# Performance work log

Measured on AMD Instinct MI355X. Metric: run time of the kernel, lower is better.

The kernel has to match this reference:

```python
import jax, jax.numpy as jnp
import numpy as np

B, L, W, C = 16, 200, 64, 128
H_INTRA = 64   # intra_hidden // 2 per direction
H_INTER = 128
EPS = 1e-8


def layer_norm(x, gamma, beta):
    mu = jnp.mean(x, axis=-1, keepdims=True)
    var = jnp.mean(jnp.square(x - mu), axis=-1, keepdims=True)
    return (x - mu) * jax.lax.rsqrt(var + EPS) * gamma + beta


def gru_seq(x, Wk, Uk, b, H):
    """Keras GRU, reset_after=False, recurrent_activation=sigmoid. x: [N,T,D] -> [N,T,H]."""
    xw = jnp.einsum('ntd,dk->ntk', x, Wk) + b  # precompute input projections [N,T,3H]
    def step(h, xw_t):
        z = jax.nn.sigmoid(xw_t[:, :H] + h @ Uk[:, :H])
        r = jax.nn.sigmoid(xw_t[:, H:2 * H] + h @ Uk[:, H:2 * H])
        hh = jnp.tanh(xw_t[:, 2 * H:] + (r * h) @ Uk[:, 2 * H:])
        h = z * h + (1.0 - z) * hh
        return h, h
    h0 = jnp.zeros((x.shape[0], H), x.dtype)
    _, ys = jax.lax.scan(step, h0, jnp.swapaxes(xw, 0, 1))  # [T,N,H]
    return jnp.swapaxes(ys, 0, 1)


def skip_gru_seq(x, Wk, Uk, b, Wp, bp, H):
    """Skip-RNN GRU (Campos et al.): binary update gate u_t conditionally updates state.
    Returns (outputs [N,T,H], gates [N,T,1])."""
    xw = jnp.einsum('ntd,dk->ntk', x, Wk) + b
    def step(carry, xw_t):
        h, ut = carry
        # straight-through binarization of cumulative update prob
        u = ut + jax.lax.stop_gradient(jnp.round(ut) - ut)  # [N,1]
        z = jax.nn.sigmoid(xw_t[:, :H] + h @ Uk[:, :H])
        r = jax.nn.sigmoid(xw_t[:, H:2 * H] + h @ Uk[:, H:2 * H])
        hh = jnp.tanh(xw_t[:, 2 * H:] + (r * h) @ Uk[:, 2 * H:])
        h_new = z * h + (1.0 - z) * hh
        h = u * h_new + (1.0 - u) * h  # skip: copy state when u == 0
        delta = jax.nn.sigmoid(h @ Wp + bp)  # [N,1]
        ut_next = u * delta + (1.0 - u) * (ut + jnp.minimum(delta, 1.0 - ut))
        return (h, ut_next), (h, u)
    N = x.shape[0]
    h0 = jnp.zeros((N, H), x.dtype)
    ut0 = jnp.ones((N, 1), x.dtype)
    _, (ys, us) = jax.lax.scan(step, (h0, ut0), jnp.swapaxes(xw, 0, 1))
    return jnp.swapaxes(ys, 0, 1), jnp.swapaxes(us, 0, 1)


def setup_inputs():
    key = jax.random.key(0)
    ks = jax.random.split(key, 16)
    rn = lambda k, s: jax.random.normal(k, s, dtype=jnp.float32) * 0.05
    z = lambda s: jnp.zeros(s, jnp.float32)
    o = lambda s: jnp.ones(s, jnp.float32)
    return {
        'x': jax.random.normal(ks[0], (B, L, W, C), dtype=jnp.float32),
        'scale': jax.random.uniform(ks[1], (B, L, W, 1), dtype=jnp.float32),
        'Wf': rn(ks[2], (C, 3 * H_INTRA)), 'Uf': rn(ks[3], (H_INTRA, 3 * H_INTRA)), 'bf': z((3 * H_INTRA,)),
        'Wb': rn(ks[4], (C, 3 * H_INTRA)), 'Ub': rn(ks[5], (H_INTRA, 3 * H_INTRA)), 'bb': z((3 * H_INTRA,)),
        'W_intra_fc': rn(ks[6], (2 * H_INTRA, C)), 'b_intra_fc': z((C,)),
        'g_intra': o((C,)), 'beta_intra': z((C,)),
        'Wi': rn(ks[7], (C + 1, 3 * H_INTER)), 'Ui': rn(ks[8], (H_INTER, 3 * H_INTER)), 'bi': z((3 * H_INTER,)),
        'Wp': rn(ks[9], (H_INTER, 1)), 'bp': z((1,)),
        'W_inter_fc': rn(ks[10], (H_INTER, C)), 'b_inter_fc': z((C,)),
        'g_inter': o((C,)), 'beta_inter': z((C,)),
    }


def reference(x, scale, Wf, Uf, bf, Wb, Ub, bb, W_intra_fc, b_intra_fc, g_intra, beta_intra,
              Wi, Ui, bi, Wp, bp, W_inter_fc, b_inter_fc, g_inter, beta_inter):
    # ----- intra path: bidirectional GRU over the width axis -----
    intra_in = x.reshape(B * L, W, C)
    out_f = gru_seq(intra_in, Wf, Uf, bf, H_INTRA)
    out_b = gru_seq(intra_in[:, ::-1, :], Wb, Ub, bb, H_INTRA)[:, ::-1, :]
    intra_rnn_out = jnp.concatenate([out_f, out_b], axis=-1)  # [B*L, W, 2H]
    update_gate_intra = jnp.ones((64, L), jnp.float32)  # skip=0 branch: constant ones
    intra_dense = intra_rnn_out @ W_intra_fc + b_intra_fc  # [B*L, W, C]
    intra_out = x + layer_norm(intra_dense.reshape(B, L, W, C), g_intra, beta_intra)
    # ----- inter path: skip-GRU over the L (time) axis -----
    inter_in = jnp.transpose(intra_out, (0, 2, 1, 3)).reshape(B * W, L, C)
    scale2 = jnp.transpose(scale, (0, 2, 1, 3)).reshape(B * W, L, 1)
    inter_in = jnp.concatenate([inter_in, scale2], axis=-1)  # [B*W, L, C+1]
    inter_rnn_out, gates = skip_gru_seq(inter_in, Wi, Ui, bi, Wp, bp, H_INTER)
    update_gate_inter = gates[:, :, 0]  # [B*W, L]
    inter_dense = (inter_rnn_out @ W_inter_fc + b_inter_fc).reshape(B, W, L, C)
    inter_ln_in = jnp.transpose(inter_dense, (0, 2, 1, 3))  # [B, L, W, C]
    inter_out = intra_out + layer_norm(inter_ln_in, g_inter, beta_inter)
    return inter_out, update_gate_intra, update_gate_inter
```

## Files before the change

kernel.cpp:

```cpp
#include <hip/hip_runtime.h>
#include <cmath>


typedef float f32x16 __attribute__((ext_vector_type(16)));

__device__ __forceinline__ float sigf(float x) { return 1.0f / (1.0f + expf(-x)); }
__device__ __forceinline__ float rlanef(float v, int l) {
  return __uint_as_float(__builtin_amdgcn_readlane(__float_as_uint(v), (unsigned)l));
}

template <int SB>
__device__ __forceinline__ void macP2(const f32x16& u0, const f32x16& u1, float hv,
                                      float& a0, float& a1) {
#pragma unroll
  for (int k = 0; k < 16; ++k) {
    const float hs = rlanef(hv, SB + k);
    a0 = fmaf(u0[k], hs, a0);
    a1 = fmaf(u1[k], hs, a1);
  }
}
template <int SB>
__device__ __forceinline__ void macP1(const f32x16& u, float hv, float& a) {
#pragma unroll
  for (int k = 0; k < 16; ++k) a = fmaf(u[k], rlanef(hv, SB + k), a);
}

__global__ __launch_bounds__(256) void k_fill_ones(float* __restrict__ p, int n) {
  int i = blockIdx.x * 256 + threadIdx.x;
  if (i < n) p[i] = 1.0f;
}

enum { MA_X_FWD = 0, MA_X_BWD = 1, MA_INTER = 2 };

template <int MODE>
__global__ __launch_bounds__(256) void k_gemm_xw(
    const float* __restrict__ A0, const float* __restrict__ A1,
    const float* __restrict__ Bm, const float* __restrict__ bias,
    float* __restrict__ Cm, long M0, int N, int K, int KT)
{
  __shared__ float As[16][68];
  __shared__ float Bs[16][68];
  const int tid = threadIdx.x;
  const int tx = tid & 15, ty = tid >> 4;
  const long row0g = M0 + (long)blockIdx.x * 64;
  const int col0 = blockIdx.y * 64;
  const int lr = tid >> 2;
  const int lk4 = (tid & 3) * 4;
  const int bk = tid >> 4;
  const int bc4 = (tid & 15) * 4;
  float acc[4][4];
#pragma unroll
  for (int i = 0; i < 4; ++i)
#pragma unroll
    for (int j = 0; j < 4; ++j) acc[i][j] = 0.f;

  for (int kt = 0; kt < KT; ++kt) {
    const int k0 = kt * 16;
    {
      const long rg = row0g + lr;
      float v0, v1, v2, v3;
      if (MODE == MA_X_FWD) {
        const float4 a4 = *reinterpret_cast<const float4*>(&A0[rg * 128 + k0 + lk4]);
        v0 = a4.x; v1 = a4.y; v2 = a4.z; v3 = a4.w;
      } else if (MODE == MA_X_BWD) {
        const long s = rg >> 6; const int t = (int)(rg & 63);
        const float4 a4 =
            *reinterpret_cast<const float4*>(&A0[(s * 64 + (63 - t)) * 128 + k0 + lk4]);
        v0 = a4.x; v1 = a4.y; v2 = a4.z; v3 = a4.w;
      } else {
        const int n = (int)(rg & 1023);
        const int l = (int)(rg >> 10);
        const long rowc = ((long)(n >> 6) * 200 + l) * 64 + (n & 63);
        const long base = rowc * 128;
        if (kt < 8) {
          const float4 a4 = *reinterpret_cast<const float4*>(&A0[base + k0 + lk4]);
          v0 = a4.x; v1 = a4.y; v2 = a4.z; v3 = a4.w;
        } else {
          v0 = (lk4 == 0) ? A1[rowc] : 0.f;
          v1 = 0.f; v2 = 0.f; v3 = 0.f;
        }
      }
      As[lk4 + 0][lr] = v0;
      As[lk4 + 1][lr] = v1;
      As[lk4 + 2][lr] = v2;
      As[lk4 + 3][lr] = v3;
    }
    {
      const int k = k0 + bk;
      float4 b4 = make_float4(0.f, 0.f, 0.f, 0.f);
      if (k < K) b4 = *reinterpret_cast<const float4*>(&Bm[(long)k * N + col0 + bc4]);
      *reinterpret_cast<float4*>(&Bs[bk][bc4]) = b4;
    }
    __syncthreads();
#pragma unroll
    for (int kk = 0; kk < 16; ++kk) {
      const float4 a4 = *reinterpret_cast<const float4*>(&As[kk][ty * 4]);
      const float4 b4 = *reinterpret_cast<const float4*>(&Bs[kk][tx * 4]);
      const float av[4] = {a4.x, a4.y, a4.z, a4.w};
      const float bv[4] = {b4.x, b4.y, b4.z, b4.w};
#pragma unroll
      for (int i = 0; i < 4; ++i)
#pragma unroll
        for (int j = 0; j < 4; ++j) acc[i][j] = fmaf(av[i], bv[j], acc[i][j]);
    }
    __syncthreads();
  }
  const float4 bi4 = *reinterpret_cast<const float4*>(&bias[col0 + tx * 4]);
  const float bv[4] = {bi4.x, bi4.y, bi4.z, bi4.w};
#pragma unroll
  for (int i = 0; i < 4; ++i) {
    const long rl = (long)blockIdx.x * 64 + ty * 4 + i;
    float4 o;
    o.x = acc[i][0] + bv[0];
    o.y = acc[i][1] + bv[1];
    o.z = acc[i][2] + bv[2];
    o.w = acc[i][3] + bv[3];
    *reinterpret_cast<float4*>(&Cm[rl * (long)N + col0 + tx * 4]) = o;
  }
}

__global__ __launch_bounds__(256, 4) void k_gru_intra4(
    const float* __restrict__ xwf, const float* __restrict__ xwb,
    const float* __restrict__ Uf, const float* __restrict__ Ub,
    float* __restrict__ rnn)
{
  const int dir = blockIdx.y;
  const float* __restrict__ xw = dir ? xwb : xwf;
  const float* __restrict__ U  = dir ? Ub : Uf;
  __shared__ float h8[4][64], z8[4][64], rh8[4][64];
  __shared__ float pA[4][4][128];
  __shared__ float pB[4][4][64];
  const int tid = threadIdx.x;
  const int w = tid >> 6, lane = tid & 63;
  const long s0 = (long)blockIdx.x * 4;

  f32x16 uz, ur, uhh;
#pragma unroll
  for (int k = 0; k < 16; ++k) {
    const int row = (w * 16 + k) * 192;
    uz[k]  = U[row + lane];
    ur[k]  = U[row + 64 + lane];
    uhh[k] = U[row + 128 + lane];
  }
  h8[w][lane] = 0.f;
  __syncthreads();

  const long xrow0 = (s0 + w) * 64;
  float xa1 = xw[xrow0 * 192 + lane];
  float xa2 = xw[xrow0 * 192 + 64 + lane];
  float xb  = xw[xrow0 * 192 + 128 + lane];

  for (int t = 0; t < 64; ++t) {
    const int tn = (t < 63) ? t + 1 : t;
    const float xa1n = xw[(xrow0 + tn) * 192 + lane];
    const float xa2n = xw[(xrow0 + tn) * 192 + 64 + lane];
    const float xbn  = xw[(xrow0 + tn) * 192 + 128 + lane];
    {
      const float hv01 = h8[lane >> 5][w * 16 + (lane & 15)];
      const float hv23 = h8[2 + (lane >> 5)][w * 16 + (lane & 15)];
      float az0 = 0.f, ar0 = 0.f, az1 = 0.f, ar1 = 0.f;
      float az2 = 0.f, ar2 = 0.f, az3 = 0.f, ar3 = 0.f;
      macP2<0>(uz, ur, hv01, az0, ar0);
      macP2<32>(uz, ur, hv01, az1, ar1);
      macP2<0>(uz, ur, hv23, az2, ar2);
      macP2<32>(uz, ur, hv23, az3, ar3);
      pA[0][w][lane] = az0; pA[0][w][64 + lane] = ar0;
      pA[1][w][lane] = az1; pA[1][w][64 + lane] = ar1;
      pA[2][w][lane] = az2; pA[2][w][64 + lane] = ar2;
      pA[3][w][lane] = az3; pA[3][w][64 + lane] = ar3;
    }
    __syncthreads();
    {
      const float sz = pA[w][0][lane] + pA[w][1][lane] + pA[w][2][lane] +
                       pA[w][3][lane] + xa1;
      const float sr = pA[w][0][64 + lane] + pA[w][1][64 + lane] +
                       pA[w][2][64 + lane] + pA[w][3][64 + lane] + xa2;
      z8[w][lane] = sigf(sz);
      rh8[w][lane] = sigf(sr) * h8[w][lane];
    }
    __syncthreads();
    {
      const float rv01 = rh8[lane >> 5][w * 16 + (lane & 15)];
      const float rv23 = rh8[2 + (lane >> 5)][w * 16 + (lane & 15)];
      float a0 = 0.f, a1 = 0.f, a2 = 0.f, a3 = 0.f;
      macP1<0>(uhh, rv01, a0);
      macP1<32>(uhh, rv01, a1);
      macP1<0>(uhh, rv23, a2);
      macP1<32>(uhh, rv23, a3);
      pB[0][w][lane] = a0;
      pB[1][w][lane] = a1;
      pB[2][w][lane] = a2;
      pB[3][w][lane] = a3;
    }
    __syncthreads();
    {
      const float pre = pB[w][0][lane] + pB[w][1][lane] + pB[w][2][lane] +
                        pB[w][3][lane] + xb;
      const float hh = tanhf(pre);
      const float z = z8[w][lane];
      const float ho = h8[w][lane];
      const float hn = z * ho + (1.f - z) * hh;
      h8[w][lane] = hn;
      const int tt = dir ? (63 - t) : t;
      rnn[((s0 + w) * 64 + tt) * 128 + dir * 64 + lane] = hn;
    }
    __syncthreads();
    xa1 = xa1n; xa2 = xa2n; xb = xbn;
  }
}

__global__ __launch_bounds__(1024, 4) void k_gru_inter5(
    const float* __restrict__ xw, const float* __restrict__ Ui,
    const float* __restrict__ Wp, const float* __restrict__ bp,
    float* __restrict__ rnn, float* __restrict__ gates,
    float* __restrict__ hstate, float* __restrict__ ustate,
    int t0, int nt)
{
  __shared__ float h4[4][128], z4[4][128], rh4[4][128];
  __shared__ float pA[4][8][256];
  __shared__ float pB[4][8][128];
  __shared__ float uu[4], utt[4];
  const int tid = threadIdx.x;
  const int w = tid >> 6, lane = tid & 63;
  const int n0 = blockIdx.x * 4;
  const int kA = (w & 7) * 16;
  const int cH = w >> 3;

  f32x16 uzA, uzB, uh;
#pragma unroll
  for (int k = 0; k < 16; ++k) {
    const long r = (long)(kA + k) * 384;
    uzA[k] = Ui[r + cH * 128 + lane];
    uzB[k] = Ui[r + cH * 128 + 64 + lane];
    uh[k]  = Ui[r + 256 + cH * 64 + lane];
  }
  if (tid < 512) {
    const int s = tid >> 7, c = tid & 127;
    h4[s][c] = (t0 == 0) ? 0.f : hstate[(long)(n0 + s) * 128 + c];
  }
  if (tid < 4) {
    utt[tid] = (t0 == 0) ? 1.f : ustate[n0 + tid];
    uu[tid]  = (t0 == 0) ? 1.f : ustate[1024 + n0 + tid];
  }
  const float bp0 = bp[0];
  float wprA = 0.f, wprB = 0.f;
  if (w < 4) { wprA = Wp[lane]; wprB = Wp[64 + lane]; }
  __syncthreads();

  const int sC = tid >> 8;
  const int cC = tid & 255;
  float xc = xw[(long)(n0 + sC) * 384 + cC];
  float xbA = 0.f, xbB = 0.f;
  if (w < 4) {
    xbA = xw[(long)(n0 + w) * 384 + 256 + lane];
    xbB = xw[(long)(n0 + w) * 384 + 320 + lane];
  }

  for (int dl = 0; dl < nt; ++dl) {
    const float u0g = uu[0], u1g = uu[1], u2g = uu[2], u3g = uu[3];
    const bool act = (u0g + u1g + u2g + u3g) != 0.f;
    const int dn = (dl + 1 < nt) ? dl + 1 : dl;
    const float xcn = xw[((long)dn * 1024 + n0 + sC) * 384 + cC];
    float xbAn = 0.f, xbBn = 0.f;
    if (w < 4) {
      xbAn = xw[((long)dn * 1024 + n0 + w) * 384 + 256 + lane];
      xbBn = xw[((long)dn * 1024 + n0 + w) * 384 + 320 + lane];
    }
    if (act) {
      {
        const float hv01 = h4[lane >> 5][kA + (lane & 15)];
        const float hv23 = h4[2 + (lane >> 5)][kA + (lane & 15)];
        const int kq = w & 7;
        if (u0g != 0.f) {
          float a0 = 0.f, a1 = 0.f;
          macP2<0>(uzA, uzB, hv01, a0, a1);
          pA[0][kq][cH * 128 + lane] = a0;
          pA[0][kq][cH * 128 + 64 + lane] = a1;
        }
        if (u1g != 0.f) {
          float a0 = 0.f, a1 = 0.f;
          macP2<32>(uzA, uzB, hv01, a0, a1);
          pA[1][kq][cH * 128 + lane] = a0;
          pA[1][kq][cH * 128 + 64 + lane] = a1;
        }
        if (u2g != 0.f) {
          float a0 = 0.f, a1 = 0.f;
          macP2<0>(uzA, uzB, hv23, a0, a1);
          pA[2][kq][cH * 128 + lane] = a0;
          pA[2][kq][cH * 128 + 64 + lane] = a1;
        }
        if (u3g != 0.f) {
          float a0 = 0.f, a1 = 0.f;
          macP2<32>(uzA, uzB, hv23, a0, a1);
          pA[3][kq][cH * 128 + lane] = a0;
          pA[3][kq][cH * 128 + 64 + lane] = a1;
        }
      }
      __syncthreads();
      {
        if (uu[sC] != 0.f) {
          float sum = xc;
#pragma unroll
          for (int q = 0; q < 8; ++q) sum += pA[sC][q][cC];
          if (cC < 128) z4[sC][cC] = sigf(sum);
          else rh4[sC][cC - 128] = sigf(sum) * h4[sC][cC - 128];
        }
      }
      __syncthreads();
      {
        const float rv01 = rh4[lane >> 5][kA + (lane & 15)];
        const float rv23 = rh4[2 + (lane >> 5)][kA + (lane & 15)];
        const int kq = w & 7;
        if (u0g != 0.f) {
          float b = 0.f; macP1<0>(uh, rv01, b);
          pB[0][kq][cH * 64 + lane] = b;
        }
        if (u1g != 0.f) {
          float b = 0.f; macP1<32>(uh, rv01, b);
          pB[1][kq][cH * 64 + lane] = b;
        }
        if (u2g != 0.f) {
          float b = 0.f; macP1<0>(uh, rv23, b);
          pB[2][kq][cH * 64 + lane] = b;
        }
        if (u3g != 0.f) {
          float b = 0.f; macP1<32>(uh, rv23, b);
          pB[3][kq][cH * 64 + lane] = b;
        }
      }
      __syncthreads();
    }
    if (w < 4) {
      const float us = uu[w];
      const float hoA = h4[w][lane], hoB = h4[w][64 + lane];
      float hqA, hqB;
      if (us != 0.f) {
        float sA = xbA, sB = xbB;
#pragma unroll
        for (int q = 0; q < 8; ++q) {
          sA += pB[w][q][lane];
          sB += pB[w][q][64 + lane];
        }
        const float hhA = tanhf(sA), hhB = tanhf(sB);
        const float zA = z4[w][lane], zB = z4[w][64 + lane];
        hqA = zA * hoA + (1.f - zA) * hhA;
        hqB = zB * hoB + (1.f - zB) * hhB;
        h4[w][lane] = hqA;
        h4[w][64 + lane] = hqB;
      } else {
        hqA = hoA; hqB = hoB;
      }
      rnn[((long)dl * 1024 + n0 + w) * 128 + lane] = hqA;
      rnn[((long)dl * 1024 + n0 + w) * 128 + 64 + lane] = hqB;
      float p = hqA * wprA + hqB * wprB;
      p += __shfl_xor(p, 32);
      p += __shfl_xor(p, 16);
      p += __shfl_xor(p, 8);
      p += __shfl_xor(p, 4);
      p += __shfl_xor(p, 2);
      p += __shfl_xor(p, 1);
      const float delta = sigf(p + bp0);
      const float ut = utt[w];
      const float utn = us * delta + (1.f - us) * (ut + fminf(delta, 1.f - ut));
      if (lane == 0) {
        gates[(long)(n0 + w) * 200 + t0 + dl] = us;
        utt[w] = utn;
        uu[w] = rintf(utn);
      }
    }
    __syncthreads();
    xc = xcn; xbA = xbAn; xbB = xbBn;
  }
  if (tid < 512) {
    const int s = tid >> 7, c = tid & 127;
    hstate[(long)(n0 + s) * 128 + c] = h4[s][c];
  }
  if (tid < 4) {
    ustate[n0 + tid] = utt[tid];
    ustate[1024 + n0 + tid] = uu[tid];
  }
}

template <int OM>
__global__ __launch_bounds__(256) void k_fcln(
    const float* __restrict__ A, const float* __restrict__ Wt,
    const float* __restrict__ bias, const float* __restrict__ gamma,
    const float* __restrict__ beta, const float* __restrict__ resid,
    float* __restrict__ dst, long M0)
{
  __shared__ float As[16][36];
  __shared__ float Bs[16][132];
  __shared__ float red0[32][33];
  __shared__ float red1[32][33];
  __shared__ float mu_s[32];
  __shared__ float rs_s[32];
  const int tid = threadIdx.x;
  const int tx = tid & 31, ty = tid >> 5;
  const long r0l = (long)blockIdx.x * 32;
  const int lr = tid >> 3;
  const int lk2 = (tid & 7) * 2;
  const int bkk = tid >> 4;
  const int bc8 = (tid & 15) * 8;
  float acc[4][4];
#pragma unroll
  for (int i = 0; i < 4; ++i)
#pragma unroll
    for (int j = 0; j < 4; ++j) acc[i][j] = 0.f;

  for (int kt = 0; kt < 8; ++kt) {
    const int k0 = kt * 16;
    const float2 a2 = *reinterpret_cast<const float2*>(&A[(r0l + lr) * 128 + k0 + lk2]);
    As[lk2][lr] = a2.x;
    As[lk2 + 1][lr] = a2.y;
    const float4 w0 = *reinterpret_cast<const float4*>(&Wt[(long)(k0 + bkk) * 128 + bc8]);
    const float4 w1 = *reinterpret_cast<const float4*>(&Wt[(long)(k0 + bkk) * 128 + bc8 + 4]);
    *reinterpret_cast<float4*>(&Bs[bkk][bc8]) = w0;
    *reinterpret_cast<float4*>(&Bs[bkk][bc8 + 4]) = w1;
    __syncthreads();
#pragma unroll
    for (int kk = 0; kk < 16; ++kk) {
      const float4 a4 = *reinterpret_cast<const float4*>(&As[kk][ty * 4]);
      const float4 b4 = *reinterpret_cast<const float4*>(&Bs[kk][tx * 4]);
      const float av[4] = {a4.x, a4.y, a4.z, a4.w};
      const float bv[4] = {b4.x, b4.y, b4.z, b4.w};
#pragma unroll
      for (int i = 0; i < 4; ++i)
#pragma unroll
        for (int j = 0; j < 4; ++j) acc[i][j] = fmaf(av[i], bv[j], acc[i][j]);
    }
    __syncthreads();
  }
  {
    const float4 bb4 = *reinterpret_cast<const float4*>(&bias[tx * 4]);
    const float bv[4] = {bb4.x, bb4.y, bb4.z, bb4.w};
#pragma unroll
    for (int i = 0; i < 4; ++i)
#pragma unroll
      for (int j = 0; j < 4; ++j) acc[i][j] += bv[j];
  }
#pragma unroll
  for (int i = 0; i < 4; ++i) {
    const float s = acc[i][0] + acc[i][1] + acc[i][2] + acc[i][3];
    const float q = acc[i][0] * acc[i][0] + acc[i][1] * acc[i][1] +
                    acc[i][2] * acc[i][2] + acc[i][3] * acc[i][3];
    red0[ty * 4 + i][tx] = s;
    red1[ty * 4 + i][tx] = q;
  }
  __syncthreads();
  if (tid < 32) {
    float s = 0.f, q = 0.f;
#pragma unroll
    for (int j = 0; j < 32; ++j) { s += red0[tid][j]; q += red1[tid][j]; }
    const float mu = s * (1.0f / 128.0f);
    const float var = q * (1.0f / 128.0f) - mu * mu;
    mu_s[tid] = mu;
    rs_s[tid] = 1.0f / sqrtf(var + 1e-8f);
  }
  __syncthreads();
  const float4 g4 = *reinterpret_cast<const float4*>(&gamma[tx * 4]);
  const float4 be4 = *reinterpret_cast<const float4*>(&beta[tx * 4]);
#pragma unroll
  for (int i = 0; i < 4; ++i) {
    const int rloc = ty * 4 + i;
    const long rg = M0 + r0l + rloc;
    long off;
    if (OM == 0) {
      off = rg * 128 + tx * 4;
    } else {
      const int n = (int)(rg & 1023);
      const int l = (int)(rg >> 10);
      off = (((long)(n >> 6) * 200 + l) * 64 + (n & 63)) * 128 + tx * 4;
    }
    const float4 r4 = *reinterpret_cast<const float4*>(&resid[off]);
    const float mu = mu_s[rloc], rs = rs_s[rloc];
    float4 o;
    o.x = (acc[i][0] - mu) * rs * g4.x + be4.x + r4.x;
    o.y = (acc[i][1] - mu) * rs * g4.y + be4.y + r4.y;
    o.z = (acc[i][2] - mu) * rs * g4.z + be4.z + r4.z;
    o.w = (acc[i][3] - mu) * rs * g4.w + be4.w + r4.w;
    *reinterpret_cast<float4*>(&dst[off]) = o;
  }
}

extern "C" void kernel_launch(void* const* d_in, const int* in_sizes, int n_in,
                              void* d_out, int out_size, void* d_ws, size_t ws_size,
                              hipStream_t stream)
{
  (void)in_sizes; (void)n_in; (void)out_size;
  const float* x    = (const float*)d_in[0];
  const float* scl  = (const float*)d_in[1];
  const float* Wf   = (const float*)d_in[2];
  const float* Uf   = (const float*)d_in[3];
  const float* bf   = (const float*)d_in[4];
  const float* Wb   = (const float*)d_in[5];
  const float* Ub   = (const float*)d_in[6];
  const float* bb   = (const float*)d_in[7];
  const float* Wfc1 = (const float*)d_in[8];
  const float* bfc1 = (const float*)d_in[9];
  const float* gam1 = (const float*)d_in[10];
  const float* bet1 = (const float*)d_in[11];
  const float* Wi   = (const float*)d_in[12];
  const float* Ui   = (const float*)d_in[13];
  const float* bi   = (const float*)d_in[14];
  const float* Wp   = (const float*)d_in[15];
  const float* bp   = (const float*)d_in[16];
  const float* Wfc2 = (const float*)d_in[17];
  const float* bfc2 = (const float*)d_in[18];
  const float* gam2 = (const float*)d_in[19];
  const float* bet2 = (const float*)d_in[20];

  float* outp  = (float*)d_out;
  float* io    = outp;
  float* onesp = outp + 26214400L;
  float* gates = outp + 26214400L + 12800L;
  float* ws    = (float*)d_ws;
  const long wsf = (long)(ws_size / sizeof(float));

  k_fill_ones<<<50, 256, 0, stream>>>(onesp, 12800);

  long cnI = (wsf / 32768L) & ~7L;
  if (cnI > 3200) cnI = 3200;
  if (cnI < 8) cnI = 8;
  for (long s0 = 0; s0 < 3200; s0 += cnI) {
    const long cn = (3200 - s0 < cnI) ? (3200 - s0) : cnI;
    float* xwf = ws;
    float* xwb = ws + cn * 12288L;
    float* rnn = ws + cn * 24576L;
    const long M = cn * 64;
    dim3 gg((unsigned)(M / 64), 3);
    k_gemm_xw<MA_X_FWD><<<gg, 256, 0, stream>>>(x, nullptr, Wf, bf, xwf, s0 * 64, 192, 128, 8);
    k_gemm_xw<MA_X_BWD><<<gg, 256, 0, stream>>>(x, nullptr, Wb, bb, xwb, s0 * 64, 192, 128, 8);
    dim3 gr((unsigned)(cn / 4), 2);
    k_gru_intra4<<<gr, 256, 0, stream>>>(xwf, xwb, Uf, Ub, rnn);
    k_fcln<0><<<(unsigned)(M / 32), 256, 0, stream>>>(rnn, Wfc1, bfc1, gam1, bet1, x, io, s0 * 64);
  }

  const long per_t = 1024L * 384 + 1024L * 128;
  const long state_f = 1024L * 128 + 3072L;
  long nt_alloc = (wsf - state_f) / per_t;
  if (nt_alloc > 200) nt_alloc = 200;
  if (nt_alloc < 1) nt_alloc = 1;
  float* xwi    = ws;
  float* rnnI   = ws + nt_alloc * 1024L * 384;
  float* hstate = rnnI + nt_alloc * 1024L * 128;
  float* ustate = hstate + 1024L * 128;

  for (long t0 = 0; t0 < 200; t0 += nt_alloc) {
    const int nt = (int)((200 - t0 < nt_alloc) ? (200 - t0) : nt_alloc);
    dim3 gg((unsigned)(16 * nt), 6);
    k_gemm_xw<MA_INTER><<<gg, 256, 0, stream>>>(io, scl, Wi, bi, xwi, t0 * 1024, 384, 129, 9);
    k_gru_inter5<<<256, 1024, 0, stream>>>(xwi, Ui, Wp, bp, rnnI, gates, hstate, ustate,
                                           (int)t0, nt);
    k_fcln<1><<<(unsigned)(32 * nt), 256, 0, stream>>>(rnnI, Wfc2, bfc2, gam2, bet2, io, outp,
                                                       t0 * 1024);
  }
}
```

Measured before the change: 1.792 ms.

## Split inter skip-GRU across 512 blocks of two sequences and widen GEMM K-tile

The inter skip-GRU kernel now handles 2 sequences per 1024-thread block instead of 4, launching 512 blocks. Each wave owns 8 rows of the recurrent matrix across all output columns, and partial sums are reduced over 16 waves. This spreads the serial recurrence over twice as many CUs to cut per-step latency, at the cost of more shared-memory reduction work and a larger register footprint per thread. Separately, the input-projection GEMM moves from a 16-wide to a 32-wide K tile, halving the number of barrier-separated iterations, and its address computation is hoisted out of the K loop.

```diff
diff --git a/kernel.cpp b/kernel.cpp
--- a/kernel.cpp
+++ b/kernel.cpp
@@ -2,29 +2,13 @@
 #include <cmath>
 
 
-typedef float f32x16 __attribute__((ext_vector_type(16)));
+typedef float f32x8 __attribute__((ext_vector_type(8)));
 
 __device__ __forceinline__ float sigf(float x) { return 1.0f / (1.0f + expf(-x)); }
 __device__ __forceinline__ float rlanef(float v, int l) {
   return __uint_as_float(__builtin_amdgcn_readlane(__float_as_uint(v), (unsigned)l));
 }
 
-template <int SB>
-__device__ __forceinline__ void macP2(const f32x16& u0, const f32x16& u1, float hv,
-                                      float& a0, float& a1) {
-#pragma unroll
-  for (int k = 0; k < 16; ++k) {
-    const float hs = rlanef(hv, SB + k);
-    a0 = fmaf(u0[k], hs, a0);
-    a1 = fmaf(u1[k], hs, a1);
-  }
-}
-template <int SB>
-__device__ __forceinline__ void macP1(const f32x16& u, float hv, float& a) {
-#pragma unroll
-  for (int k = 0; k < 16; ++k) a = fmaf(u[k], rlanef(hv, SB + k), a);
-}
-
 __global__ __launch_bounds__(256) void k_fill_ones(float* __restrict__ p, int n) {
   int i = blockIdx.x * 256 + threadIdx.x;
   if (i < n) p[i] = 1.0f;
@@ -33,13 +17,13 @@
 enum { MA_X_FWD = 0, MA_X_BWD = 1, MA_INTER = 2 };
 
 template <int MODE>
-__global__ __launch_bounds__(256) void k_gemm_xw(
+__global__ __launch_bounds__(256, 6) void k_gemm_xw(
     const float* __restrict__ A0, const float* __restrict__ A1,
     const float* __restrict__ Bm, const float* __restrict__ bias,
     float* __restrict__ Cm, long M0, int N, int K, int KT)
 {
-  __shared__ float As[16][68];
-  __shared__ float Bs[16][68];
+  __shared__ float As[32][68];
+  __shared__ float Bs[32][68];
   const int tid = threadIdx.x;
   const int tx = tid & 15, ty = tid >> 4;
   const long row0g = M0 + (long)blockIdx.x * 64;
@@ -54,46 +38,54 @@
 #pragma unroll
     for (int j = 0; j < 4; ++j) acc[i][j] = 0.f;
 
+  const long rg = row0g + lr;
+  long abase = 0;
+  long rowc = 0;
+  if (MODE == MA_X_FWD) {
+    abase = rg * 128;
+  } else if (MODE == MA_X_BWD) {
+    const long s = rg >> 6; const int t = (int)(rg & 63);
+    abase = (s * 64 + (63 - t)) * 128;
+  } else {
+    const int n = (int)(rg & 1023);
+    const int l = (int)(rg >> 10);
+    rowc = ((long)(n >> 6) * 200 + l) * 64 + (n & 63);
+    abase = rowc * 128;
+  }
+
   for (int kt = 0; kt < KT; ++kt) {
-    const int k0 = kt * 16;
-    {
-      const long rg = row0g + lr;
+    const int k0 = kt * 32;
+#pragma unroll
+    for (int half = 0; half < 32; half += 16) {
+      const int kk0 = k0 + half + lk4;
       float v0, v1, v2, v3;
-      if (MODE == MA_X_FWD) {
-        const float4 a4 = *reinterpret_cast<const float4*>(&A0[rg * 128 + k0 + lk4]);
-        v0 = a4.x; v1 = a4.y; v2 = a4.z; v3 = a4.w;
-      } else if (MODE == MA_X_BWD) {
-        const long s = rg >> 6; const int t = (int)(rg & 63);
-        const float4 a4 =
-            *reinterpret_cast<const float4*>(&A0[(s * 64 + (63 - t)) * 128 + k0 + lk4]);
+      if (MODE != MA_INTER || kk0 + 3 < 128) {
+        const float4 a4 = *reinterpret_cast<const float4*>(&A0[abase + kk0]);
         v0 = a4.x; v1 = a4.y; v2 = a4.z; v3 = a4.w;
       } else {
-        const int n = (int)(rg & 1023);
-        const int l = (int)(rg >> 10);
-        const long rowc = ((long)(n >> 6) * 200 + l) * 64 + (n & 63);
-        const long base = rowc * 128;
-        if (kt < 8) {
-          const float4 a4 = *reinterpret_cast<const float4*>(&A0[base + k0 + lk4]);
-          v0 = a4.x; v1 = a4.y; v2 = a4.z; v3 = a4.w;
-        } else {
-          v0 = (lk4 == 0) ? A1[rowc] : 0.f;
-          v1 = 0.f; v2 = 0.f; v3 = 0.f;
-        }
+        float vv[4];
+#pragma unroll
+        for (int i = 0; i < 4; ++i) {
+          const int k = kk0 + i;
+          vv[i] = (k < 128) ? A0[abase + k] : ((k == 128) ? A1[rowc] : 0.f);
+        }
+        v0 = vv[0]; v1 = vv[1]; v2 = vv[2]; v3 = vv[3];
       }
-      As[lk4 + 0][lr] = v0;
-      As[lk4 + 1][lr] = v1;
-      As[lk4 + 2][lr] = v2;
-      As[lk4 + 3][lr] = v3;
-    }
-    {
-      const int k = k0 + bk;
+      As[half + lk4 + 0][lr] = v0;
+      As[half + lk4 + 1][lr] = v1;
+      As[half + lk4 + 2][lr] = v2;
+      As[half + lk4 + 3][lr] = v3;
+    }
+#pragma unroll
+    for (int half = 0; half < 32; half += 16) {
+      const int k = k0 + half + bk;
       float4 b4 = make_float4(0.f, 0.f, 0.f, 0.f);
       if (k < K) b4 = *reinterpret_cast<const float4*>(&Bm[(long)k * N + col0 + bc4]);
-      *reinterpret_cast<float4*>(&Bs[bk][bc4]) = b4;
-    }
-    __syncthreads();
-#pragma unroll
-    for (int kk = 0; kk < 16; ++kk) {
+      *reinterpret_cast<float4*>(&Bs[half + bk][bc4]) = b4;
+    }
+    __syncthreads();
+#pragma unroll
+    for (int kk = 0; kk < 32; ++kk) {
       const float4 a4 = *reinterpret_cast<const float4*>(&As[kk][ty * 4]);
       const float4 b4 = *reinterpret_cast<const float4*>(&Bs[kk][tx * 4]);
       const float av[4] = {a4.x, a4.y, a4.z, a4.w};
@@ -117,6 +109,23 @@
     o.w = acc[i][3] + bv[3];
     *reinterpret_cast<float4*>(&Cm[rl * (long)N + col0 + tx * 4]) = o;
   }
+}
+
+typedef float f32x16 __attribute__((ext_vector_type(16)));
+template <int SB>
+__device__ __forceinline__ void macP2(const f32x16& u0, const f32x16& u1, float hv,
+                                      float& a0, float& a1) {
+#pragma unroll
+  for (int k = 0; k < 16; ++k) {
+    const float hs = rlanef(hv, SB + k);
+    a0 = fmaf(u0[k], hs, a0);
+    a1 = fmaf(u1[k], hs, a1);
+  }
+}
+template <int SB>
+__device__ __forceinline__ void macP1(const f32x16& u, float hv, float& a) {
+#pragma unroll
+  for (int k = 0; k < 16; ++k) a = fmaf(u[k], rlanef(hv, SB + k), a);
 }
 
 __global__ __launch_bounds__(256, 4) void k_gru_intra4(
@@ -209,135 +218,142 @@
   }
 }
 
-__global__ __launch_bounds__(1024, 4) void k_gru_inter5(
+__global__ __launch_bounds__(1024, 8) void k_gru_inter6(
     const float* __restrict__ xw, const float* __restrict__ Ui,
     const float* __restrict__ Wp, const float* __restrict__ bp,
     float* __restrict__ rnn, float* __restrict__ gates,
     float* __restrict__ hstate, float* __restrict__ ustate,
     int t0, int nt)
 {
-  __shared__ float h4[4][128], z4[4][128], rh4[4][128];
-  __shared__ float pA[4][8][256];
-  __shared__ float pB[4][8][128];
-  __shared__ float uu[4], utt[4];
+  __shared__ float h4[2][128], z4[2][128], rh4[2][128];
+  __shared__ float pA[2][16][256];
+  __shared__ float pB[2][16][128];
+  __shared__ float uu[2], utt[2];
   const int tid = threadIdx.x;
   const int w = tid >> 6, lane = tid & 63;
-  const int n0 = blockIdx.x * 4;
-  const int kA = (w & 7) * 16;
-  const int cH = w >> 3;
-
-  f32x16 uzA, uzB, uh;
-#pragma unroll
-  for (int k = 0; k < 16; ++k) {
-    const long r = (long)(kA + k) * 384;
-    uzA[k] = Ui[r + cH * 128 + lane];
-    uzB[k] = Ui[r + cH * 128 + 64 + lane];
-    uh[k]  = Ui[r + 256 + cH * 64 + lane];
-  }
-  if (tid < 512) {
+  const int w8 = w << 3;
+  const int n0 = blockIdx.x * 2;
+
+  f32x8 u0, u1, u2, u3;
+  f32x8 v0, v1;
+#pragma unroll
+  for (int k = 0; k < 8; ++k) {
+    const long r = (long)(w8 + k) * 384;
+    u0[k] = Ui[r + lane];
+    u1[k] = Ui[r + 64 + lane];
+    u2[k] = Ui[r + 128 + lane];
+    u3[k] = Ui[r + 192 + lane];
+    v0[k] = Ui[r + 256 + lane];
+    v1[k] = Ui[r + 256 + 64 + lane];
+  }
+  if (tid < 256) {
     const int s = tid >> 7, c = tid & 127;
     h4[s][c] = (t0 == 0) ? 0.f : hstate[(long)(n0 + s) * 128 + c];
   }
-  if (tid < 4) {
+  if (tid < 2) {
     utt[tid] = (t0 == 0) ? 1.f : ustate[n0 + tid];
     uu[tid]  = (t0 == 0) ? 1.f : ustate[1024 + n0 + tid];
   }
   const float bp0 = bp[0];
-  float wprA = 0.f, wprB = 0.f;
-  if (w < 4) { wprA = Wp[lane]; wprB = Wp[64 + lane]; }
+  float wpA = 0.f, wpB = 0.f;
+  if (w < 2) { wpA = Wp[lane]; wpB = Wp[64 + lane]; }
   __syncthreads();
 
   const int sC = tid >> 8;
   const int cC = tid & 255;
-  float xc = xw[(long)(n0 + sC) * 384 + cC];
-  float xbA = 0.f, xbB = 0.f;
-  if (w < 4) {
+  float xc = 0.f, xbA = 0.f, xbB = 0.f;
+  if (tid < 512) xc = xw[(long)(n0 + sC) * 384 + cC];
+  if (w < 2) {
     xbA = xw[(long)(n0 + w) * 384 + 256 + lane];
     xbB = xw[(long)(n0 + w) * 384 + 320 + lane];
   }
 
   for (int dl = 0; dl < nt; ++dl) {
-    const float u0g = uu[0], u1g = uu[1], u2g = uu[2], u3g = uu[3];
-    const bool act = (u0g + u1g + u2g + u3g) != 0.f;
+    const float u0g = uu[0], u1g = uu[1];
+    const bool act = (u0g + u1g) != 0.f;
     const int dn = (dl + 1 < nt) ? dl + 1 : dl;
-    const float xcn = xw[((long)dn * 1024 + n0 + sC) * 384 + cC];
-    float xbAn = 0.f, xbBn = 0.f;
-    if (w < 4) {
+    float xcn = 0.f, xbAn = 0.f, xbBn = 0.f;
+    if (tid < 512) xcn = xw[((long)dn * 1024 + n0 + sC) * 384 + cC];
+    if (w < 2) {
       xbAn = xw[((long)dn * 1024 + n0 + w) * 384 + 256 + lane];
       xbBn = xw[((long)dn * 1024 + n0 + w) * 384 + 320 + lane];
     }
     if (act) {
       {
-        const float hv01 = h4[lane >> 5][kA + (lane & 15)];
-        const float hv23 = h4[2 + (lane >> 5)][kA + (lane & 15)];
-        const int kq = w & 7;
         if (u0g != 0.f) {
-          float a0 = 0.f, a1 = 0.f;
-          macP2<0>(uzA, uzB, hv01, a0, a1);
-          pA[0][kq][cH * 128 + lane] = a0;
-          pA[0][kq][cH * 128 + 64 + lane] = a1;
+          const float hv = h4[0][w8 + (lane & 7)];
+          float a0 = 0.f, a1 = 0.f, a2 = 0.f, a3 = 0.f;
+#pragma unroll
+          for (int j = 0; j < 8; ++j) {
+            const float hs = rlanef(hv, j);
+            a0 = fmaf(u0[j], hs, a0);
+            a1 = fmaf(u1[j], hs, a1);
+            a2 = fmaf(u2[j], hs, a2);
+            a3 = fmaf(u3[j], hs, a3);
+          }
+          pA[0][w][lane] = a0; pA[0][w][64 + lane] = a1;
+          pA[0][w][128 + lane] = a2; pA[0][w][192 + lane] = a3;
         }
         if (u1g != 0.f) {
-          float a0 = 0.f, a1 = 0.f;
-          macP2<32>(uzA, uzB, hv01, a0, a1);
-          pA[1][kq][cH * 128 + lane] = a0;
-          pA[1][kq][cH * 128 + 64 + lane] = a1;
-        }
-        if (u2g != 0.f) {
-          float a0 = 0.f, a1 = 0.f;
-          macP2<0>(uzA, uzB, hv23, a0, a1);
-          pA[2][kq][cH * 128 + lane] = a0;
-          pA[2][kq][cH * 128 + 64 + lane] = a1;
-        }
-        if (u3g != 0.f) {
-          float a0 = 0.f, a1 = 0.f;
-          macP2<32>(uzA, uzB, hv23, a0, a1);
-          pA[3][kq][cH * 128 + lane] = a0;
-          pA[3][kq][cH * 128 + 64 + lane] = a1;
+          const float hv = h4[1][w8 + (lane & 7)];
+          float a0 = 0.f, a1 = 0.f, a2 = 0.f, a3 = 0.f;
+#pragma unroll
+          for (int j = 0; j < 8; ++j) {
+            const float hs = rlanef(hv, j);
+            a0 = fmaf(u0[j], hs, a0);
+            a1 = fmaf(u1[j], hs, a1);
+            a2 = fmaf(u2[j], hs, a2);
+            a3 = fmaf(u3[j], hs, a3);
+          }
+          pA[1][w][lane] = a0; pA[1][w][64 + lane] = a1;
+          pA[1][w][128 + lane] = a2; pA[1][w][192 + lane] = a3;
+        }
+      }
+      __syncthreads();
+      if (tid < 512) {
+        if (uu[sC] != 0.f) {
+          float sum = xc;
+#pragma unroll
+          for (int q = 0; q < 16; ++q) sum += pA[sC][q][cC];
+          if (cC < 128) z4[sC][cC] = sigf(sum);
+          else rh4[sC][cC - 128] = sigf(sum) * h4[sC][cC - 128];
         }
       }
       __syncthreads();
       {
-        if (uu[sC] != 0.f) {
-          float sum = xc;
-#pragma unroll
-          for (int q = 0; q < 8; ++q) sum += pA[sC][q][cC];
-          if (cC < 128) z4[sC][cC] = sigf(sum);
-          else rh4[sC][cC - 128] = sigf(sum) * h4[sC][cC - 128];
+        if (u0g != 0.f) {
+          const float rv = rh4[0][w8 + (lane & 7)];
+          float b0 = 0.f, b1 = 0.f;
+#pragma unroll
+          for (int j = 0; j < 8; ++j) {
+            const float rs = rlanef(rv, j);
+            b0 = fmaf(v0[j], rs, b0);
+            b1 = fmaf(v1[j], rs, b1);
+          }
+          pB[0][w][lane] = b0; pB[0][w][64 + lane] = b1;
+        }
+        if (u1g != 0.f) {
+          const float rv = rh4[1][w8 + (lane & 7)];
+          float b0 = 0.f, b1 = 0.f;
+#pragma unroll
+          for (int j = 0; j < 8; ++j) {
+            const float rs = rlanef(rv, j);
+            b0 = fmaf(v0[j], rs, b0);
+            b1 = fmaf(v1[j], rs, b1);
+          }
+          pB[1][w][lane] = b0; pB[1][w][64 + lane] = b1;
         }
       }
       __syncthreads();
-      {
-        const float rv01 = rh4[lane >> 5][kA + (lane & 15)];
-        const float rv23 = rh4[2 + (lane >> 5)][kA + (lane & 15)];
-        const int kq = w & 7;
-        if (u0g != 0.f) {
-          float b = 0.f; macP1<0>(uh, rv01, b);
-          pB[0][kq][cH * 64 + lane] = b;
-        }
-        if (u1g != 0.f) {
-          float b = 0.f; macP1<32>(uh, rv01, b);
-          pB[1][kq][cH * 64 + lane] = b;
-        }
-        if (u2g != 0.f) {
-          float b = 0.f; macP1<0>(uh, rv23, b);
-          pB[2][kq][cH * 64 + lane] = b;
-        }
-        if (u3g != 0.f) {
-          float b = 0.f; macP1<32>(uh, rv23, b);
-          pB[3][kq][cH * 64 + lane] = b;
-        }
-      }
-      __syncthreads();
-    }
-    if (w < 4) {
+    }
+    if (w < 2) {
       const float us = uu[w];
       const float hoA = h4[w][lane], hoB = h4[w][64 + lane];
       float hqA, hqB;
       if (us != 0.f) {
         float sA = xbA, sB = xbB;
 #pragma unroll
-        for (int q = 0; q < 8; ++q) {
+        for (int q = 0; q < 16; ++q) {
           sA += pB[w][q][lane];
           sB += pB[w][q][64 + lane];
         }
@@ -352,18 +368,18 @@
       }
       rnn[((long)dl * 1024 + n0 + w) * 128 + lane] = hqA;
       rnn[((long)dl * 1024 + n0 + w) * 128 + 64 + lane] = hqB;
-      float p = hqA * wprA + hqB * wprB;
+      float p = hqA * wpA + hqB * wpB;
       p += __shfl_xor(p, 32);
       p += __shfl_xor(p, 16);
       p += __shfl_xor(p, 8);
       p += __shfl_xor(p, 4);
       p += __shfl_xor(p, 2);
       p += __shfl_xor(p, 1);
-      const float delta = sigf(p + bp0);
-      const float ut = utt[w];
-      const float utn = us * delta + (1.f - us) * (ut + fminf(delta, 1.f - ut));
       if (lane == 0) {
+        const float delta = sigf(p + bp0);
+        const float ut = utt[w];
         gates[(long)(n0 + w) * 200 + t0 + dl] = us;
+        const float utn = us * delta + (1.f - us) * (ut + fminf(delta, 1.f - ut));
         utt[w] = utn;
         uu[w] = rintf(utn);
       }
@@ -371,11 +387,11 @@
     __syncthreads();
     xc = xcn; xbA = xbAn; xbB = xbBn;
   }
-  if (tid < 512) {
+  if (tid < 256) {
     const int s = tid >> 7, c = tid & 127;
     hstate[(long)(n0 + s) * 128 + c] = h4[s][c];
   }
-  if (tid < 4) {
+  if (tid < 2) {
     ustate[n0 + tid] = utt[tid];
     ustate[1024 + n0 + tid] = uu[tid];
   }
@@ -528,8 +544,8 @@
     float* rnn = ws + cn * 24576L;
     const long M = cn * 64;
     dim3 gg((unsigned)(M / 64), 3);
-    k_gemm_xw<MA_X_FWD><<<gg, 256, 0, stream>>>(x, nullptr, Wf, bf, xwf, s0 * 64, 192, 128, 8);
-    k_gemm_xw<MA_X_BWD><<<gg, 256, 0, stream>>>(x, nullptr, Wb, bb, xwb, s0 * 64, 192, 128, 8);
+    k_gemm_xw<MA_X_FWD><<<gg, 256, 0, stream>>>(x, nullptr, Wf, bf, xwf, s0 * 64, 192, 128, 4);
+    k_gemm_xw<MA_X_BWD><<<gg, 256, 0, stream>>>(x, nullptr, Wb, bb, xwb, s0 * 64, 192, 128, 4);
     dim3 gr((unsigned)(cn / 4), 2);
     k_gru_intra4<<<gr, 256, 0, stream>>>(xwf, xwb, Uf, Ub, rnn);
     k_fcln<0><<<(unsigned)(M / 32), 256, 0, stream>>>(rnn, Wfc1, bfc1, gam1, bet1, x, io, s0 * 64);
@@ -548,8 +564,8 @@
   for (long t0 = 0; t0 < 200; t0 += nt_alloc) {
     const int nt = (int)((200 - t0 < nt_alloc) ? (200 - t0) : nt_alloc);
     dim3 gg((unsigned)(16 * nt), 6);
-    k_gemm_xw<MA_INTER><<<gg, 256, 0, stream>>>(io, scl, Wi, bi, xwi, t0 * 1024, 384, 129, 9);
-    k_gru_inter5<<<256, 1024, 0, stream>>>(xwi, Ui, Wp, bp, rnnI, gates, hstate, ustate,
+    k_gemm_xw<MA_INTER><<<gg, 256, 0, stream>>>(io, scl, Wi, bi, xwi, t0 * 1024, 384, 129, 5);
+    k_gru_inter6<<<512, 1024, 0, stream>>>(xwi, Ui, Wp, bp, rnnI, gates, hstate, ustate,
                                            (int)t0, nt);
     k_fcln<1><<<(unsigned)(32 * nt), 256, 0, stream>>>(rnnI, Wfc2, bfc2, gam2, bet2, io, outp,
                                                        t0 * 1024);
```

New measurement: 3.686 ms. 106% more time.
